# Optimization experiments

Hardware: AMD Instinct MI355X
Metric: run time of the kernel (lower is better)

## Reference

```python
import jax, jax.numpy as jnp
import numpy as np

RMS_EPS = 1e-6
B, S, H = 2, 4096, 4096
N_Q_OUT, N_KV_OUT = 4096, 1024  # 32 heads * 128, 8 kv heads * 128


def setup_inputs() -> dict:
    key = jax.random.key(0)
    k1, k2, k3, k4 = jax.random.split(key, 4)
    scale = 1.0 / np.sqrt(H)
    return {
        "hidden_states": jax.random.normal(k1, (B, S, H), dtype=jnp.float32),
        "gamma": jnp.ones((H,), dtype=jnp.float32),
        "w_q": jax.random.normal(k2, (H, N_Q_OUT), dtype=jnp.float32) * scale,
        "w_k": jax.random.normal(k3, (H, N_KV_OUT), dtype=jnp.float32) * scale,
        "w_v": jax.random.normal(k4, (H, N_KV_OUT), dtype=jnp.float32) * scale,
    }


def _rmsnorm(x, gamma, eps=RMS_EPS):
    # x: [B, S, H]; normalize over last axis
    var = jnp.mean(jnp.square(x), axis=-1, keepdims=True)
    return x * jax.lax.rsqrt(var + eps) * gamma


def reference(hidden_states, gamma, w_q, w_k, w_v):
    # Fused RMSNorm + QKV projection (GQA): normalize once, then three
    # column-parallel matmuls sharing the normalized activation.
    xn = _rmsnorm(hidden_states, gamma)  # [B, S, H]
    q = jnp.einsum("bsh,hd->bsd", xn, w_q)  # [B, S, n_heads*head_dim]
    k = jnp.einsum("bsh,hd->bsd", xn, w_k)  # [B, S, n_kv_heads*head_dim]
    v = jnp.einsum("bsh,hd->bsd", xn, w_v)  # [B, S, n_kv_heads*head_dim]
    return q, k, v
```

## Files before the change

### kernel.cpp

```cpp
#include <hip/hip_runtime.h>
#include <hip/hip_bf16.h>
#include <stdint.h>

#define HD      4096
#define MROWS   8192
#define NQ      4096
#define NKV     1024
#define NTOT    6144
#define RMS_EPS 1e-6f

typedef __attribute__((ext_vector_type(8))) short bf16x8;
typedef __attribute__((ext_vector_type(4))) float f32x4;

static __device__ __forceinline__ unsigned short f2bf(float f) {
  union { float f; unsigned u; } a; a.f = f;
  unsigned r = a.u + 0x7FFFu + ((a.u >> 16) & 1u);
  return (unsigned short)(r >> 16);
}

__global__ __launch_bounds__(256) void rmsnorm_cast_kernel(
    const float* __restrict__ x, const float* __restrict__ gamma,
    unsigned short* __restrict__ xn) {
  const int row = blockIdx.x;
  const float4* xr = (const float4*)(x + (size_t)row * HD);
  const float4* g4 = (const float4*)gamma;
  const int t = threadIdx.x;
  float4 v[4];
  float ss = 0.f;
#pragma unroll
  for (int i = 0; i < 4; ++i) {
    v[i] = xr[t + i * 256];
    ss += v[i].x * v[i].x + v[i].y * v[i].y + v[i].z * v[i].z + v[i].w * v[i].w;
  }
#pragma unroll
  for (int o = 32; o > 0; o >>= 1) ss += __shfl_xor(ss, o, 64);
  __shared__ float red[4];
  if ((t & 63) == 0) red[t >> 6] = ss;
  __syncthreads();
  const float tot = red[0] + red[1] + red[2] + red[3];
  const float rstd = rsqrtf(tot * (1.f / HD) + RMS_EPS);
  ushort4* xo = (ushort4*)(xn + (size_t)row * HD);
#pragma unroll
  for (int i = 0; i < 4; ++i) {
    const float4 g = g4[t + i * 256];
    ushort4 o;
    o.x = f2bf(v[i].x * rstd * g.x);
    o.y = f2bf(v[i].y * rstd * g.y);
    o.z = f2bf(v[i].z * rstd * g.z);
    o.w = f2bf(v[i].w * rstd * g.w);
    xo[t + i * 256] = o;
  }
}

__global__ __launch_bounds__(256) void transpose_cast_kernel(
    const float* __restrict__ w, unsigned short* __restrict__ wt, int Nw) {
  __shared__ float tile[32][33];
  const int kt = blockIdx.y;
  const int nb = blockIdx.x;
  const int t = threadIdx.x;
  const int r = t >> 3, c4 = t & 7;
  const float4 vin = *(const float4*)&w[(size_t)(kt * 32 + r) * Nw + nb * 32 + c4 * 4];
  tile[r][c4 * 4 + 0] = vin.x;
  tile[r][c4 * 4 + 1] = vin.y;
  tile[r][c4 * 4 + 2] = vin.z;
  tile[r][c4 * 4 + 3] = vin.w;
  __syncthreads();
  ushort4 o;
  o.x = f2bf(tile[c4 * 4 + 0][r]);
  o.y = f2bf(tile[c4 * 4 + 1][r]);
  o.z = f2bf(tile[c4 * 4 + 2][r]);
  o.w = f2bf(tile[c4 * 4 + 3][r]);
  *(ushort4*)&wt[(size_t)(nb * 32 + r) * HD + kt * 32 + c4 * 4] = o;
}


static __device__ __forceinline__ void gload_lds16(const unsigned short* g,
                                                   unsigned short* l) {
  __builtin_amdgcn_global_load_lds(
      (const __attribute__((address_space(1))) void*)g,
      (__attribute__((address_space(3))) void*)l, 16, 0, 0);
}

#define VM4 asm volatile("s_waitcnt vmcnt(4)" ::: "memory")
#define VM0 asm volatile("s_waitcnt vmcnt(0)" ::: "memory")
#define VMNONE ((void)0)

#define READS_A(BUF, HA)                                                       \
  do {                                                                         \
    const unsigned short* Ah = &lds[0][BUF][HA][0];                            \
    _Pragma("unroll") for (int im = 0; im < 4; ++im) {                         \
      const int r = wr * 64 + im * 16 + fr;                                    \
      af[im][0] = *(const bf16x8*)((const char*)Ah + r * 128 + kb0);           \
      af[im][1] = *(const bf16x8*)((const char*)Ah + r * 128 + (kb0 ^ 64));    \
    }                                                                          \
  } while (0)

#define READS_B(BUF, HB)                                                       \
  do {                                                                         \
    const unsigned short* Bh = &lds[1][BUF][HB][0];                            \
    _Pragma("unroll") for (int jn = 0; jn < 2; ++jn) {                         \
      const int rb = wc * 32 + jn * 16 + fr;                                   \
      bfr[jn][0] = *(const bf16x8*)((const char*)Bh + rb * 128 + kb0);         \
      bfr[jn][1] = *(const bf16x8*)((const char*)Bh + rb * 128 + (kb0 ^ 64));  \
    }                                                                          \
  } while (0)

#define MMA(HA, HB, VM)                                                        \
  do {                                                                         \
    __builtin_amdgcn_s_barrier();                                              \
    __builtin_amdgcn_s_setprio(1);                                             \
    _Pragma("unroll") for (int ks = 0; ks < 2; ++ks)                           \
      _Pragma("unroll") for (int im = 0; im < 4; ++im)                         \
        _Pragma("unroll") for (int jn = 0; jn < 2; ++jn)                       \
          acc[(HA) * 4 + im][(HB) * 2 + jn] =                                  \
              __builtin_amdgcn_mfma_f32_16x16x32_bf16(                         \
                  af[im][ks], bfr[jn][ks], acc[(HA) * 4 + im][(HB) * 2 + jn],  \
                  0, 0, 0);                                                    \
    __builtin_amdgcn_s_setprio(0);                                             \
    VM;                                                                        \
    __builtin_amdgcn_s_barrier();                                              \
  } while (0)

#define PAIR(BUF, HA, STG1, VM1, STG2, VM2)                                    \
  do {                                                                         \
    READS_A(BUF, HA);                                                          \
    READS_B(BUF, 0);                                                           \
    STG1;                                                                      \
    MMA(HA, 0, VM1);                                                           \
    READS_B(BUF, 1);                                                           \
    STG2;                                                                      \
    MMA(HA, 1, VM2);                                                           \
  } while (0)

__global__ __launch_bounds__(512, 2) void gemm_qkv_kernel(
    const unsigned short* __restrict__ A,
    const unsigned short* __restrict__ Bt,
    float* __restrict__ out) {
  __shared__ unsigned short lds[2][2][2][8192] __attribute__((aligned(16)));

  const int bid = blockIdx.x;
  const int xcd = bid & 7;
  const int idx = bid >> 3;
  const int sr  = idx >> 5;
  const int i32 = idx & 31;
  const int mt  = (xcd >> 1) * 8 + (i32 >> 2);
  const int nt  = (xcd & 1) * 12 + sr * 4 + (i32 & 3);
  const int m0 = mt * 256, n0 = nt * 256;

  const int tid = threadIdx.x;
  const int w = tid >> 6, lane = tid & 63;
  const int wr = w >> 2, wc = w & 3;
  const int fr = lane & 15, fq = lane >> 4;
  const int kb0 = ((lane >> 4) << 4) ^ ((fr & 7) << 4);

  const int wslot = w * 512;
  const int r3 = tid >> 3;
  const int scolb = ((tid & 7) << 4) ^ ((r3 & 7) << 4);
  const size_t so0 = (size_t)r3 * HD + (scolb >> 1);
  const size_t so1 = so0 + (size_t)64 * HD;

  const unsigned short* const Ab0 = A + (size_t)m0 * HD;
  const unsigned short* const Ab1 = Ab0 + (size_t)128 * HD;
  const unsigned short* const Bb0 = Bt + (size_t)n0 * HD;
  const unsigned short* const Bb1 = Bb0 + (size_t)128 * HD;

  auto STG = [&](const unsigned short* g, unsigned short* l) {
    gload_lds16(g + so0, l + wslot);
    gload_lds16(g + so1, l + 4096 + wslot);
  };

  f32x4 acc[8][4];
#pragma unroll
  for (int i = 0; i < 8; ++i)
#pragma unroll
    for (int j = 0; j < 4; ++j) acc[i][j] = (f32x4){0.f, 0.f, 0.f, 0.f};

  bf16x8 af[4][2];
  bf16x8 bfr[2][2];

  STG(Ab0, &lds[0][0][0][0]);
  STG(Bb0, &lds[1][0][0][0]);
  STG(Ab1, &lds[0][0][1][0]);
  STG(Bb1, &lds[1][0][1][0]);
  STG(Ab0 + 64, &lds[0][1][0][0]);
  STG(Bb0 + 64, &lds[1][1][0][0]);
  VM4;
  __builtin_amdgcn_s_barrier();

  for (int t = 0; t < 31; ++t) {
    const size_t k1 = (size_t)(2 * t + 1) * 64;
    const size_t o2 = (size_t)(2 * t + 2) * 64;
    const size_t o3 = (size_t)(2 * t + 3) * 64;
    PAIR(0, 0, STG(Ab1 + k1, &lds[0][1][1][0]), VMNONE,
               STG(Bb1 + k1, &lds[1][1][1][0]), VMNONE);
    PAIR(0, 1, STG(Ab0 + o2, &lds[0][0][0][0]), VMNONE,
               STG(Bb0 + o2, &lds[1][0][0][0]), VM4);
    PAIR(1, 0, STG(Ab1 + o2, &lds[0][0][1][0]), VMNONE,
               STG(Bb1 + o2, &lds[1][0][1][0]), VMNONE);
    PAIR(1, 1, STG(Ab0 + o3, &lds[0][1][0][0]), VMNONE,
               STG(Bb0 + o3, &lds[1][1][0][0]), VM4);
  }
  {
    const size_t k1 = (size_t)63 * 64;
    PAIR(0, 0, STG(Ab1 + k1, &lds[0][1][1][0]), VMNONE,
               STG(Bb1 + k1, &lds[1][1][1][0]), VMNONE);
    PAIR(0, 1, VMNONE, VMNONE, VMNONE, VM0);
    PAIR(1, 0, VMNONE, VMNONE, VMNONE, VMNONE);
    PAIR(1, 1, VMNONE, VMNONE, VMNONE, VMNONE);
  }

  size_t obase; int ldc, nc;
  if (n0 < NQ)            { obase = 0;                                        ldc = NQ;  nc = n0; }
  else if (n0 < NQ + NKV) { obase = (size_t)MROWS * NQ;                       ldc = NKV; nc = n0 - NQ; }
  else                    { obase = (size_t)MROWS * NQ + (size_t)MROWS * NKV; ldc = NKV; nc = n0 - NQ - NKV; }

#pragma unroll
  for (int I = 0; I < 8; ++I) {
    const int rown = m0 + (I >> 2) * 128 + wr * 64 + (I & 3) * 16 + fq * 4;
#pragma unroll
    for (int J = 0; J < 4; ++J) {
      const int col = nc + (J >> 1) * 128 + wc * 32 + (J & 1) * 16 + fr;
#pragma unroll
      for (int jj = 0; jj < 4; ++jj)
        out[obase + (size_t)(rown + jj) * ldc + col] = acc[I][J][jj];
    }
  }
}

extern "C" void kernel_launch(void* const* d_in, const int* in_sizes, int n_in,
                              void* d_out, int out_size, void* d_ws, size_t ws_size,
                              hipStream_t stream) {
  const float* x     = (const float*)d_in[0];
  const float* gamma = (const float*)d_in[1];
  const float* wq    = (const float*)d_in[2];
  const float* wk    = (const float*)d_in[3];
  const float* wv    = (const float*)d_in[4];
  float* out = (float*)d_out;

  unsigned short* xn = (unsigned short*)d_ws;
  unsigned short* wt = xn + (size_t)MROWS * HD;

  rmsnorm_cast_kernel<<<MROWS, 256, 0, stream>>>(x, gamma, xn);
  transpose_cast_kernel<<<dim3(NQ / 32, HD / 32), 256, 0, stream>>>(wq, wt, NQ);
  transpose_cast_kernel<<<dim3(NKV / 32, HD / 32), 256, 0, stream>>>(
      wk, wt + (size_t)NQ * HD, NKV);
  transpose_cast_kernel<<<dim3(NKV / 32, HD / 32), 256, 0, stream>>>(
      wv, wt + (size_t)(NQ + NKV) * HD, NKV);
  gemm_qkv_kernel<<<(MROWS / 256) * (NTOT / 256), 512, 0, stream>>>(xn, wt, out);
}
```

Before: 409.9 us.

## Switch GEMM to 32x32x16 MFMA with reordered LDS read/stage schedule

Replaces the 16x16x32 bf16 MFMA tiles with 32x32x16 MFMA instructions. This changes the accumulator layout, the fragment loads and the LDS swizzle so that B fragments are reused across two A fragments. The per-pair schedule becomes a serpentine order over sub-tiles, interleaving LDS reads and global-to-LDS staging, which cuts LDS read traffic per MFMA. The risk is that the different swizzle may cause bank conflicts, and the stores of the larger accumulator tiles are less contiguous.

```diff
diff --git a/kernel.cpp b/kernel.cpp
--- a/kernel.cpp
+++ b/kernel.cpp
@@ -10,7 +10,7 @@
 #define RMS_EPS 1e-6f
 
 typedef __attribute__((ext_vector_type(8))) short bf16x8;
-typedef __attribute__((ext_vector_type(4))) float f32x4;
+typedef __attribute__((ext_vector_type(16))) float f32x16;
 
 static __device__ __forceinline__ unsigned short f2bf(float f) {
   union { float f; unsigned u; } a; a.f = f;
@@ -85,51 +85,34 @@
 #define VM0 asm volatile("s_waitcnt vmcnt(0)" ::: "memory")
 #define VMNONE ((void)0)
 
-#define READS_A(BUF, HA)                                                       \
+#define RD_A(BUF, HA)                                                          \
   do {                                                                         \
-    const unsigned short* Ah = &lds[0][BUF][HA][0];                            \
-    _Pragma("unroll") for (int im = 0; im < 4; ++im) {                         \
-      const int r = wr * 64 + im * 16 + fr;                                    \
-      af[im][0] = *(const bf16x8*)((const char*)Ah + r * 128 + kb0);           \
-      af[im][1] = *(const bf16x8*)((const char*)Ah + r * 128 + (kb0 ^ 64));    \
-    }                                                                          \
+    const char* Ah = (const char*)&lds[0][BUF][HA][0];                         \
+    _Pragma("unroll") for (int mi = 0; mi < 2; ++mi)                           \
+      _Pragma("unroll") for (int ks = 0; ks < 4; ++ks)                         \
+        af[mi][ks] = *(const bf16x8*)(Ah + (wr * 64 + mi * 32 + r32) * 128 +   \
+                                      (((ks * 2 + hi) ^ swx) << 4));           \
   } while (0)
 
-#define READS_B(BUF, HB)                                                       \
+#define RD_B(BUF, HB)                                                          \
   do {                                                                         \
-    const unsigned short* Bh = &lds[1][BUF][HB][0];                            \
-    _Pragma("unroll") for (int jn = 0; jn < 2; ++jn) {                         \
-      const int rb = wc * 32 + jn * 16 + fr;                                   \
-      bfr[jn][0] = *(const bf16x8*)((const char*)Bh + rb * 128 + kb0);         \
-      bfr[jn][1] = *(const bf16x8*)((const char*)Bh + rb * 128 + (kb0 ^ 64));  \
-    }                                                                          \
+    const char* Bh = (const char*)&lds[1][BUF][HB][0];                         \
+    _Pragma("unroll") for (int ks = 0; ks < 4; ++ks)                           \
+      bfr[ks] = *(const bf16x8*)(Bh + (wc * 32 + r32) * 128 +                  \
+                                 (((ks * 2 + hi) ^ swx) << 4));                \
   } while (0)
 
 #define MMA(HA, HB, VM)                                                        \
   do {                                                                         \
     __builtin_amdgcn_s_barrier();                                              \
     __builtin_amdgcn_s_setprio(1);                                             \
-    _Pragma("unroll") for (int ks = 0; ks < 2; ++ks)                           \
-      _Pragma("unroll") for (int im = 0; im < 4; ++im)                         \
-        _Pragma("unroll") for (int jn = 0; jn < 2; ++jn)                       \
-          acc[(HA) * 4 + im][(HB) * 2 + jn] =                                  \
-              __builtin_amdgcn_mfma_f32_16x16x32_bf16(                         \
-                  af[im][ks], bfr[jn][ks], acc[(HA) * 4 + im][(HB) * 2 + jn],  \
-                  0, 0, 0);                                                    \
+    _Pragma("unroll") for (int ks = 0; ks < 4; ++ks)                           \
+      _Pragma("unroll") for (int mi = 0; mi < 2; ++mi)                         \
+        acc[(HA) * 2 + mi][HB] = __builtin_amdgcn_mfma_f32_32x32x16_bf16(      \
+            af[mi][ks], bfr[ks], acc[(HA) * 2 + mi][HB], 0, 0, 0);             \
     __builtin_amdgcn_s_setprio(0);                                             \
     VM;                                                                        \
     __builtin_amdgcn_s_barrier();                                              \
-  } while (0)
-
-#define PAIR(BUF, HA, STG1, VM1, STG2, VM2)                                    \
-  do {                                                                         \
-    READS_A(BUF, HA);                                                          \
-    READS_B(BUF, 0);                                                           \
-    STG1;                                                                      \
-    MMA(HA, 0, VM1);                                                           \
-    READS_B(BUF, 1);                                                           \
-    STG2;                                                                      \
-    MMA(HA, 1, VM2);                                                           \
   } while (0)
 
 __global__ __launch_bounds__(512, 2) void gemm_qkv_kernel(
@@ -150,12 +133,12 @@
   const int tid = threadIdx.x;
   const int w = tid >> 6, lane = tid & 63;
   const int wr = w >> 2, wc = w & 3;
-  const int fr = lane & 15, fq = lane >> 4;
-  const int kb0 = ((lane >> 4) << 4) ^ ((fr & 7) << 4);
+  const int r32 = lane & 31, hi = lane >> 5;
+  const int swx = (r32 >> 2) & 7;
 
   const int wslot = w * 512;
   const int r3 = tid >> 3;
-  const int scolb = ((tid & 7) << 4) ^ ((r3 & 7) << 4);
+  const int scolb = (((tid & 7) ^ ((r3 >> 2) & 7))) << 4;
   const size_t so0 = (size_t)r3 * HD + (scolb >> 1);
   const size_t so1 = so0 + (size_t)64 * HD;
 
@@ -169,14 +152,14 @@
     gload_lds16(g + so1, l + 4096 + wslot);
   };
 
-  f32x4 acc[8][4];
-#pragma unroll
-  for (int i = 0; i < 8; ++i)
-#pragma unroll
-    for (int j = 0; j < 4; ++j) acc[i][j] = (f32x4){0.f, 0.f, 0.f, 0.f};
-
-  bf16x8 af[4][2];
-  bf16x8 bfr[2][2];
+  f32x16 acc[4][2];
+#pragma unroll
+  for (int i = 0; i < 4; ++i)
+#pragma unroll
+    for (int j = 0; j < 2; ++j) acc[i][j] = (f32x16)(0.f);
+
+  bf16x8 af[2][4];
+  bf16x8 bfr[4];
 
   STG(Ab0, &lds[0][0][0][0]);
   STG(Bb0, &lds[1][0][0][0]);
@@ -191,22 +174,25 @@
     const size_t k1 = (size_t)(2 * t + 1) * 64;
     const size_t o2 = (size_t)(2 * t + 2) * 64;
     const size_t o3 = (size_t)(2 * t + 3) * 64;
-    PAIR(0, 0, STG(Ab1 + k1, &lds[0][1][1][0]), VMNONE,
-               STG(Bb1 + k1, &lds[1][1][1][0]), VMNONE);
-    PAIR(0, 1, STG(Ab0 + o2, &lds[0][0][0][0]), VMNONE,
-               STG(Bb0 + o2, &lds[1][0][0][0]), VM4);
-    PAIR(1, 0, STG(Ab1 + o2, &lds[0][0][1][0]), VMNONE,
-               STG(Bb1 + o2, &lds[1][0][1][0]), VMNONE);
-    PAIR(1, 1, STG(Ab0 + o3, &lds[0][1][0][0]), VMNONE,
-               STG(Bb0 + o3, &lds[1][1][0][0]), VM4);
+    RD_A(0, 0); RD_B(0, 1); STG(Bb1 + k1, &lds[1][1][1][0]); MMA(0, 1, VMNONE);
+    RD_B(0, 0);             STG(Ab1 + k1, &lds[0][1][1][0]); MMA(0, 0, VMNONE);
+    RD_A(0, 1);             STG(Bb0 + o2, &lds[1][0][0][0]); MMA(1, 0, VMNONE);
+    RD_B(0, 1);             STG(Ab1 + o2, &lds[0][0][1][0]); MMA(1, 1, VM4);
+    RD_A(1, 0); RD_B(1, 1); STG(Ab0 + o2, &lds[0][0][0][0]); MMA(0, 1, VMNONE);
+    RD_B(1, 0);             STG(Bb1 + o2, &lds[1][0][1][0]); MMA(0, 0, VMNONE);
+    RD_A(1, 1);             STG(Ab0 + o3, &lds[0][1][0][0]); MMA(1, 0, VMNONE);
+    RD_B(1, 1);             STG(Bb0 + o3, &lds[1][1][0][0]); MMA(1, 1, VM4);
   }
   {
     const size_t k1 = (size_t)63 * 64;
-    PAIR(0, 0, STG(Ab1 + k1, &lds[0][1][1][0]), VMNONE,
-               STG(Bb1 + k1, &lds[1][1][1][0]), VMNONE);
-    PAIR(0, 1, VMNONE, VMNONE, VMNONE, VM0);
-    PAIR(1, 0, VMNONE, VMNONE, VMNONE, VMNONE);
-    PAIR(1, 1, VMNONE, VMNONE, VMNONE, VMNONE);
+    RD_A(0, 0); RD_B(0, 1); STG(Bb1 + k1, &lds[1][1][1][0]); MMA(0, 1, VMNONE);
+    RD_B(0, 0);             STG(Ab1 + k1, &lds[0][1][1][0]); MMA(0, 0, VMNONE);
+    RD_A(0, 1);                                              MMA(1, 0, VMNONE);
+    RD_B(0, 1);                                              MMA(1, 1, VM0);
+    RD_A(1, 0); RD_B(1, 1);                                  MMA(0, 1, VMNONE);
+    RD_B(1, 0);                                              MMA(0, 0, VMNONE);
+    RD_A(1, 1);                                              MMA(1, 0, VMNONE);
+    RD_B(1, 1);                                              MMA(1, 1, VMNONE);
   }
 
   size_t obase; int ldc, nc;
@@ -215,14 +201,16 @@
   else                    { obase = (size_t)MROWS * NQ + (size_t)MROWS * NKV; ldc = NKV; nc = n0 - NQ - NKV; }
 
 #pragma unroll
-  for (int I = 0; I < 8; ++I) {
-    const int rown = m0 + (I >> 2) * 128 + wr * 64 + (I & 3) * 16 + fq * 4;
-#pragma unroll
-    for (int J = 0; J < 4; ++J) {
-      const int col = nc + (J >> 1) * 128 + wc * 32 + (J & 1) * 16 + fr;
-#pragma unroll
-      for (int jj = 0; jj < 4; ++jj)
-        out[obase + (size_t)(rown + jj) * ldc + col] = acc[I][J][jj];
+  for (int I = 0; I < 4; ++I) {
+    const int rbase = m0 + (I >> 1) * 128 + wr * 64 + (I & 1) * 32 + hi * 4;
+#pragma unroll
+    for (int J = 0; J < 2; ++J) {
+      const int col = nc + J * 128 + wc * 32 + r32;
+#pragma unroll
+      for (int reg = 0; reg < 16; ++reg) {
+        const int row = rbase + (reg & 3) + 8 * (reg >> 2);
+        out[obase + (size_t)row * ldc + col] = acc[I][J][reg];
+      }
     }
   }
 }
```

After: 452.3 us. +10.4%, slower.
